# Kernel optimization log

Measured on AMD Instinct MI355X. Metric: run time of the kernel, lower is better.

## Reference

```python
import jax, jax.numpy as jnp
import numpy as np

B, C, H, T = 20, 395, 10, 8192  # batch, input channels, hidden, seq len
GATE_IN = 2 * C + H             # = 800, matches Linear(800, 10)
INIT_IN = 87                    # initilaizer = Linear(87, hidden)


def _uni(k, shape, fan_in):
    s = 1.0 / np.sqrt(fan_in)
    return jax.random.uniform(k, shape, jnp.float32, -s, s)


def setup_inputs() -> dict:
    key = jax.random.key(0)
    ks = jax.random.split(key, 12)
    x = jax.random.normal(ks[0], (B, C, T), jnp.float32)
    y = jax.random.normal(ks[1], (B, C, T), jnp.float32)
    Wf = _uni(ks[2], (H, GATE_IN), GATE_IN); bf = _uni(ks[3], (H,), GATE_IN)
    Wi = _uni(ks[4], (H, GATE_IN), GATE_IN); bi = _uni(ks[5], (H,), GATE_IN)
    Wu = _uni(ks[6], (H, GATE_IN), GATE_IN); bu = _uni(ks[7], (H,), GATE_IN)
    Wo = _uni(ks[8], (H, GATE_IN), GATE_IN); bo = _uni(ks[9], (H,), GATE_IN)
    W_init = _uni(ks[10], (H, INIT_IN), INIT_IN); b_init = _uni(ks[11], (H,), INIT_IN)
    return dict(x=x, y=y, Wf=Wf, bf=bf, Wi=Wi, bi=bi, Wu=Wu, bu=bu,
                Wo=Wo, bo=bo, W_init=W_init, b_init=b_init)


def reference(x, y, Wf, bf, Wi, bi, Wu, bu, Wo, bo, W_init, b_init):
    b_, c_, t_ = x.shape
    h_ = Wf.shape[0]
    # initial states: h0 zeros; c0 = Linear(87->H)(zeros(20,87)) == broadcast bias
    h0 = jnp.zeros((b_, h_), x.dtype)
    c0 = jnp.zeros((b_, INIT_IN), x.dtype) @ W_init.T + b_init  # (B, H)
    # y_prev[t] = y[t-1], zeros at t=0
    y_prev = jnp.concatenate([jnp.zeros((b_, c_, 1), x.dtype), y[..., :-1]], axis=-1)
    # stacked input per step is [x_t, h, y_prev]; split weights accordingly
    W = jnp.stack([Wf, Wi, Wu, Wo])           # (4, H, 2C+H)
    bvec = jnp.stack([bf, bi, bu, bo])        # (4, H)
    Wx, Wh, Wy = W[..., :c_], W[..., c_:c_ + h_], W[..., c_ + h_:]
    # precompute all input-dependent gate pre-activations: (T, B, 4, H)
    pre = (jnp.einsum('bct,ghc->tbgh', x, Wx)
           + jnp.einsum('bct,ghc->tbgh', y_prev, Wy)
           + bvec)

    def step(carry, pre_t):
        h, c = carry
        z = pre_t + jnp.einsum('bh,goh->bgo', h, Wh)  # (B, 4, H)
        f = jax.nn.sigmoid(z[:, 0])
        i = jax.nn.sigmoid(z[:, 1])
        g = jnp.tanh(z[:, 2])
        o = jax.nn.sigmoid(z[:, 3])
        c = c * f + i * g
        h = o * jnp.tanh(c)
        return (h, c), h

    (_, cT), hs = jax.lax.scan(step, (h0, c0), pre)  # hs: (T, B, H)
    out = jnp.moveaxis(hs, 0, -1)  # (B, H, T), matches torch.stack(..., dim=-1)
    return out, cT
```

## Files before the change

kernel.cpp:

```cpp
#include <hip/hip_runtime.h>

#define Bn 20
#define Cn 395
#define Hn 10
#define Tn 8192
#define TP (Tn + 8)
#define GIN 800
#define CP 400
#define NL2E (-1.4426950408889634f)

__global__ __launch_bounds__(256) void pclstm_wt(
    const float* __restrict__ Wf, const float* __restrict__ Wi,
    const float* __restrict__ Wu, const float* __restrict__ Wo,
    float* __restrict__ wt)
{
  int i = blockIdx.x * 256 + threadIdx.x;
  if (i >= CP * 80) return;
  int c = i / 80;
  int q = i - c * 80;
  float v = 0.f;
  if (c < Cn) {
    int qq = (q < 40) ? q : q - 40;
    int h = qq >> 2;
    int g = qq & 3;
    const float* W = (g == 0) ? Wf : (g == 1) ? Wi : (g == 2) ? Wu : Wo;
    float s = (g == 2) ? 2.f * NL2E : NL2E;
    int col = (q < 40) ? c : (Cn + Hn + c);
    v = W[h * GIN + col] * s;
  }
  wt[i] = v;
}

#define SC 80
#define NSTAGE (CP / SC)

__global__ __launch_bounds__(256) void pclstm_pre(
    const float* __restrict__ x, const float* __restrict__ y,
    const float* __restrict__ wt, float* __restrict__ pre)
{
  __shared__ float4 wls[SC * 20];

  const int tid = threadIdx.x;
  const int b = blockIdx.y;
  const int t = blockIdx.x * 256 + tid;

  const float* xb = x + (size_t)b * Cn * Tn + t;
  const float* yb = y + (size_t)b * Cn * Tn + ((t > 0) ? t - 1 : 0);
  const float ym = (t > 0) ? 1.f : 0.f;

  float acc[40];
#pragma unroll
  for (int q = 0; q < 40; ++q) acc[q] = 0.f;

  float xr[8], yr[8];
#pragma unroll
  for (int d = 0; d < 8; ++d) {
    xr[d] = xb[(size_t)d * Tn];
    yr[d] = ym * yb[(size_t)d * Tn];
  }

  const float4* wt4 = reinterpret_cast<const float4*>(wt);

  for (int s = 0; s < NSTAGE; ++s) {
    __syncthreads();
#pragma unroll
    for (int i = 0; i < 7; ++i) {
      int idx = i * 256 + tid;
      if (idx < SC * 20) wls[idx] = wt4[(size_t)s * (SC * 20) + idx];
    }
    __syncthreads();

#pragma unroll 8
    for (int cc = 0; cc < SC; ++cc) {
      const int c = s * SC + cc;
      const int slot = cc & 7;
      float xv = xr[slot];
      float yv = yr[slot];
      int cp = c + 8;
      cp = (cp < Cn) ? cp : (Cn - 1);
      xr[slot] = xb[(size_t)cp * Tn];
      yr[slot] = ym * yb[(size_t)cp * Tn];

      const float4* wr4 = &wls[cc * 20];
#pragma unroll
      for (int k = 0; k < 10; ++k) {
        float4 wx = wr4[k];
        float4 wy = wr4[k + 10];
        acc[4*k+0] = fmaf(xv, wx.x, acc[4*k+0]);
        acc[4*k+1] = fmaf(xv, wx.y, acc[4*k+1]);
        acc[4*k+2] = fmaf(xv, wx.z, acc[4*k+2]);
        acc[4*k+3] = fmaf(xv, wx.w, acc[4*k+3]);
        acc[4*k+0] = fmaf(yv, wy.x, acc[4*k+0]);
        acc[4*k+1] = fmaf(yv, wy.y, acc[4*k+1]);
        acc[4*k+2] = fmaf(yv, wy.z, acc[4*k+2]);
        acc[4*k+3] = fmaf(yv, wy.w, acc[4*k+3]);
      }
    }
  }

  float4* dst = reinterpret_cast<float4*>(pre + ((size_t)b * TP + t) * 40);
#pragma unroll
  for (int k = 0; k < 10; ++k) {
    float4 v4;
    v4.x = acc[4*k+0]; v4.y = acc[4*k+1]; v4.z = acc[4*k+2]; v4.w = acc[4*k+3];
    dst[k] = v4;
  }
}

#define QP(v, ctrl) __int_as_float(__builtin_amdgcn_update_dpp( \
    0, __float_as_int(v), (ctrl), 0xf, 0xf, true))

__global__ __launch_bounds__(64) void pclstm_scan(
    const float* __restrict__ pre,
    const float* __restrict__ Wf, const float* __restrict__ Wi,
    const float* __restrict__ Wu, const float* __restrict__ Wo,
    const float* __restrict__ bfp, const float* __restrict__ bip,
    const float* __restrict__ bup, const float* __restrict__ bop,
    const float* __restrict__ b_init,
    float* __restrict__ out)
{
  const int b = blockIdx.x;
  const int l = threadIdx.x;
  const int lc = (l < 40) ? l : 39;
  const int o = lc >> 2;
  const int g = lc & 3;

  const float* W  = (g == 0) ? Wf : (g == 1) ? Wi : (g == 2) ? Wu : Wo;
  const float* bp = (g == 0) ? bfp : (g == 1) ? bip : (g == 2) ? bup : bop;
  const float sg  = (g == 2) ? 2.f * NL2E : NL2E;
  const float ag  = (g == 2) ? 2.f : 1.f;
  const float bgc = (g == 2) ? -1.f : 0.f;

  float wh[10];
#pragma unroll
  for (int j = 0; j < 10; ++j) wh[j] = W[o * GIN + Cn + j] * sg;
  const float sgb = sg * bp[o];

  const float* preb = pre + (size_t)b * TP * 40 + lc;
  float c = b_init[o];
  float h = 0.f;
  float hb[10];
#pragma unroll
  for (int j = 0; j < 10; ++j) hb[j] = 0.f;

  float pbuf[8];
#pragma unroll
  for (int k = 0; k < 8; ++k) pbuf[k] = preb[(size_t)k * 40];

  const bool sl = (l < 40) && (g == 3);
  float* outb = out + (size_t)b * Hn * Tn;
  float hs[4];

#pragma unroll 8
  for (int t = 0; t < Tn; ++t) {
    float pv = pbuf[t & 7];
    pbuf[t & 7] = preb[(size_t)(t + 8) * 40];

    float pvs = pv + sgb;

    float m1 = wh[2] * hb[2];
    float m2 = wh[4] * hb[4];
    float m3 = wh[6] * hb[6];
    float m4 = wh[8] * hb[8];
    float s0 = fmaf(wh[0], hb[0], pvs);
    float s1 = fmaf(wh[1], hb[1], m1);
    float s2 = fmaf(wh[3], hb[3], m2);
    float s3 = fmaf(wh[5], hb[5], m3);
    float s4 = fmaf(wh[7], hb[7], m4);
    s0 = fmaf(wh[9], hb[9], s0);
    float zs = (s0 + s1) + (s2 + (s3 + s4));

    float e = __builtin_amdgcn_exp2f(zs);
    float r = __builtin_amdgcn_rcpf(1.f + e);
    float gate = fmaf(ag, r, bgc);

    float fv = QP(gate, 0x00);
    float iv = QP(gate, 0x55);
    float uv = QP(gate, 0xAA);
    float ov = QP(gate, 0xFF);

    c = fmaf(c, fv, iv * uv);
    float zc = (2.f * NL2E) * c;
    float e2 = __builtin_amdgcn_exp2f(zc);
    float r2 = __builtin_amdgcn_rcpf(1.f + e2);
    float th = fmaf(2.f, r2, -1.f);
    h = ov * th;

    hs[t & 3] = h;
    if (((t & 3) == 3) && sl) {
      float4 v4; v4.x = hs[0]; v4.y = hs[1]; v4.z = hs[2]; v4.w = hs[3];
      *reinterpret_cast<float4*>(outb + (size_t)o * Tn + t - 3) = v4;
    }

#pragma unroll
    for (int j = 0; j < 10; ++j)
      hb[j] = __int_as_float(__builtin_amdgcn_readlane(__float_as_int(h), 4 * j));
  }
  if ((l < 40) && (g == 0)) out[(size_t)Bn * Hn * Tn + b * Hn + o] = c;
}

extern "C" void kernel_launch(void* const* d_in, const int* in_sizes, int n_in,
                              void* d_out, int out_size, void* d_ws, size_t ws_size,
                              hipStream_t stream) {
  const float* x      = (const float*)d_in[0];
  const float* y      = (const float*)d_in[1];
  const float* Wf     = (const float*)d_in[2];
  const float* bf     = (const float*)d_in[3];
  const float* Wi     = (const float*)d_in[4];
  const float* bi     = (const float*)d_in[5];
  const float* Wu     = (const float*)d_in[6];
  const float* bu     = (const float*)d_in[7];
  const float* Wo     = (const float*)d_in[8];
  const float* bo     = (const float*)d_in[9];
  const float* b_init = (const float*)d_in[11];
  float* out = (float*)d_out;

  float* wt  = (float*)d_ws;
  float* pre = (float*)((char*)d_ws + 131072);

  pclstm_wt<<<(CP * 80 + 255) / 256, 256, 0, stream>>>(Wf, Wi, Wu, Wo, wt);
  dim3 g1(Tn / 256, Bn);
  pclstm_pre<<<g1, 256, 0, stream>>>(x, y, wt, pre);
  pclstm_scan<<<Bn, 64, 0, stream>>>(pre, Wf, Wi, Wu, Wo, bf, bi, bu, bo, b_init, out);
}
```

Before: 1.427 ms.

## Fuse projection and scan into one kernel with flag-based producer/consumer overlap

```diff
diff --git a/kernel.cpp b/kernel.cpp
--- a/kernel.cpp
+++ b/kernel.cpp
@@ -8,13 +8,20 @@
 #define GIN 800
 #define CP 400
 #define NL2E (-1.4426950408889634f)
-
-__global__ __launch_bounds__(256) void pclstm_wt(
+#define KC (2.f * NL2E)
+
+#define SUBT 128
+#define NSUB (Tn / SUBT)
+#define PREBLK (NSUB * Bn)
+#define NFLAGS (Bn * NSUB)
+
+__global__ __launch_bounds__(256) void pclstm_setup(
     const float* __restrict__ Wf, const float* __restrict__ Wi,
     const float* __restrict__ Wu, const float* __restrict__ Wo,
-    float* __restrict__ wt)
+    float* __restrict__ wt, int* __restrict__ flags)
 {
   int i = blockIdx.x * 256 + threadIdx.x;
+  if (i < NFLAGS) flags[i] = 0;
   if (i >= CP * 80) return;
   int c = i / 80;
   int q = i - c * 80;
@@ -31,87 +38,13 @@
   wt[i] = v;
 }
 
-#define SC 80
-#define NSTAGE (CP / SC)
-
-__global__ __launch_bounds__(256) void pclstm_pre(
-    const float* __restrict__ x, const float* __restrict__ y,
-    const float* __restrict__ wt, float* __restrict__ pre)
-{
-  __shared__ float4 wls[SC * 20];
-
-  const int tid = threadIdx.x;
-  const int b = blockIdx.y;
-  const int t = blockIdx.x * 256 + tid;
-
-  const float* xb = x + (size_t)b * Cn * Tn + t;
-  const float* yb = y + (size_t)b * Cn * Tn + ((t > 0) ? t - 1 : 0);
-  const float ym = (t > 0) ? 1.f : 0.f;
-
-  float acc[40];
-#pragma unroll
-  for (int q = 0; q < 40; ++q) acc[q] = 0.f;
-
-  float xr[8], yr[8];
-#pragma unroll
-  for (int d = 0; d < 8; ++d) {
-    xr[d] = xb[(size_t)d * Tn];
-    yr[d] = ym * yb[(size_t)d * Tn];
-  }
-
-  const float4* wt4 = reinterpret_cast<const float4*>(wt);
-
-  for (int s = 0; s < NSTAGE; ++s) {
-    __syncthreads();
-#pragma unroll
-    for (int i = 0; i < 7; ++i) {
-      int idx = i * 256 + tid;
-      if (idx < SC * 20) wls[idx] = wt4[(size_t)s * (SC * 20) + idx];
-    }
-    __syncthreads();
-
-#pragma unroll 8
-    for (int cc = 0; cc < SC; ++cc) {
-      const int c = s * SC + cc;
-      const int slot = cc & 7;
-      float xv = xr[slot];
-      float yv = yr[slot];
-      int cp = c + 8;
-      cp = (cp < Cn) ? cp : (Cn - 1);
-      xr[slot] = xb[(size_t)cp * Tn];
-      yr[slot] = ym * yb[(size_t)cp * Tn];
-
-      const float4* wr4 = &wls[cc * 20];
-#pragma unroll
-      for (int k = 0; k < 10; ++k) {
-        float4 wx = wr4[k];
-        float4 wy = wr4[k + 10];
-        acc[4*k+0] = fmaf(xv, wx.x, acc[4*k+0]);
-        acc[4*k+1] = fmaf(xv, wx.y, acc[4*k+1]);
-        acc[4*k+2] = fmaf(xv, wx.z, acc[4*k+2]);
-        acc[4*k+3] = fmaf(xv, wx.w, acc[4*k+3]);
-        acc[4*k+0] = fmaf(yv, wy.x, acc[4*k+0]);
-        acc[4*k+1] = fmaf(yv, wy.y, acc[4*k+1]);
-        acc[4*k+2] = fmaf(yv, wy.z, acc[4*k+2]);
-        acc[4*k+3] = fmaf(yv, wy.w, acc[4*k+3]);
-      }
-    }
-  }
-
-  float4* dst = reinterpret_cast<float4*>(pre + ((size_t)b * TP + t) * 40);
-#pragma unroll
-  for (int k = 0; k < 10; ++k) {
-    float4 v4;
-    v4.x = acc[4*k+0]; v4.y = acc[4*k+1]; v4.z = acc[4*k+2]; v4.w = acc[4*k+3];
-    dst[k] = v4;
-  }
-}
-
 #define QP(v, ctrl) __int_as_float(__builtin_amdgcn_update_dpp( \
     0, __float_as_int(v), (ctrl), 0xf, 0xf, true))
 
-__global__ __launch_bounds__(64) void pclstm_scan(
-    const float* __restrict__ pre,
+__global__ __launch_bounds__(128) void pclstm_fused(
+    const float* __restrict__ x, const float* __restrict__ y,
+    const float* __restrict__ wt, float* __restrict__ pre,
+    int* __restrict__ flags,
     const float* __restrict__ Wf, const float* __restrict__ Wi,
     const float* __restrict__ Wu, const float* __restrict__ Wo,
     const float* __restrict__ bfp, const float* __restrict__ bip,
@@ -119,84 +52,173 @@
     const float* __restrict__ b_init,
     float* __restrict__ out)
 {
-  const int b = blockIdx.x;
-  const int l = threadIdx.x;
-  const int lc = (l < 40) ? l : 39;
-  const int o = lc >> 2;
-  const int g = lc & 3;
+  __shared__ float4 wls[200 * 20];
+
+  const int bid = blockIdx.x;
+  const int tid = threadIdx.x;
+
+  if (bid >= Bn) {
+    const int i = bid - Bn;
+    const int sub = i / Bn;
+    const int b = i - sub * Bn;
+    const int t = sub * SUBT + tid;
+
+    const float* xb = x + (size_t)b * Cn * Tn + t;
+    const float* yb = y + (size_t)b * Cn * Tn + ((t > 0) ? t - 1 : 0);
+    const float ym = (t > 0) ? 1.f : 0.f;
+
+    float acc[40];
+#pragma unroll
+    for (int q = 0; q < 40; ++q) acc[q] = 0.f;
+
+    float xr[8], yr[8];
+#pragma unroll
+    for (int d = 0; d < 8; ++d) {
+      xr[d] = xb[(size_t)d * Tn];
+      yr[d] = ym * yb[(size_t)d * Tn];
+    }
+
+    const float4* wt4 = reinterpret_cast<const float4*>(wt);
+
+    for (int half = 0; half < 2; ++half) {
+      __syncthreads();
+      for (int j = tid; j < 4000; j += 128)
+        wls[j] = wt4[half * 4000 + j];
+      __syncthreads();
+
+#pragma unroll 8
+      for (int cc = 0; cc < 200; ++cc) {
+        const int c = half * 200 + cc;
+        const int slot = cc & 7;
+        float xv = xr[slot], yv = yr[slot];
+        int cp = c + 8;
+        cp = (cp < Cn) ? cp : (Cn - 1);
+        xr[slot] = xb[(size_t)cp * Tn];
+        yr[slot] = ym * yb[(size_t)cp * Tn];
+
+        const float4* wr4 = &wls[cc * 20];
+#pragma unroll
+        for (int k = 0; k < 10; ++k) {
+          float4 wx = wr4[k];
+          float4 wy = wr4[k + 10];
+          acc[4*k+0] = fmaf(xv, wx.x, acc[4*k+0]);
+          acc[4*k+1] = fmaf(xv, wx.y, acc[4*k+1]);
+          acc[4*k+2] = fmaf(xv, wx.z, acc[4*k+2]);
+          acc[4*k+3] = fmaf(xv, wx.w, acc[4*k+3]);
+          acc[4*k+0] = fmaf(yv, wy.x, acc[4*k+0]);
+          acc[4*k+1] = fmaf(yv, wy.y, acc[4*k+1]);
+          acc[4*k+2] = fmaf(yv, wy.z, acc[4*k+2]);
+          acc[4*k+3] = fmaf(yv, wy.w, acc[4*k+3]);
+        }
+      }
+    }
+
+    float4* dst = reinterpret_cast<float4*>(pre + ((size_t)b * TP + t) * 40);
+#pragma unroll
+    for (int k = 0; k < 10; ++k) {
+      float4 v4;
+      v4.x = acc[4*k+0]; v4.y = acc[4*k+1]; v4.z = acc[4*k+2]; v4.w = acc[4*k+3];
+      dst[k] = v4;
+    }
+
+    __syncthreads();
+    if (tid == 0)
+      __hip_atomic_store(&flags[b * NSUB + sub], 1,
+                         __ATOMIC_RELEASE, __HIP_MEMORY_SCOPE_AGENT);
+    return;
+  }
+
+  if (tid >= 40) return;
+  const int b = bid;
+  const int l = tid;
+  const int o = l >> 2;
+  const int g = l & 3;
 
   const float* W  = (g == 0) ? Wf : (g == 1) ? Wi : (g == 2) ? Wu : Wo;
   const float* bp = (g == 0) ? bfp : (g == 1) ? bip : (g == 2) ? bup : bop;
   const float sg  = (g == 2) ? 2.f * NL2E : NL2E;
-  const float ag  = (g == 2) ? 2.f : 1.f;
-  const float bgc = (g == 2) ? -1.f : 0.f;
+  const float ag  = (g == 2) ? 2.f * KC : 1.f;
+  const float bgc = (g == 2) ? -KC : 0.f;
 
   float wh[10];
 #pragma unroll
   for (int j = 0; j < 10; ++j) wh[j] = W[o * GIN + Cn + j] * sg;
   const float sgb = sg * bp[o];
 
-  const float* preb = pre + (size_t)b * TP * 40 + lc;
-  float c = b_init[o];
+  int* fb = flags + b * NSUB;
+  const float* preb = pre + (size_t)b * TP * 40 + l;
+  float cs = KC * b_init[o];
   float h = 0.f;
   float hb[10];
 #pragma unroll
   for (int j = 0; j < 10; ++j) hb[j] = 0.f;
 
+  while (__hip_atomic_load(&fb[0], __ATOMIC_ACQUIRE, __HIP_MEMORY_SCOPE_AGENT) == 0)
+    __builtin_amdgcn_s_sleep(2);
+
   float pbuf[8];
 #pragma unroll
   for (int k = 0; k < 8; ++k) pbuf[k] = preb[(size_t)k * 40];
 
-  const bool sl = (l < 40) && (g == 3);
+  const bool sl = (g == 3);
   float* outb = out + (size_t)b * Hn * Tn;
-  float hs[4];
-
+  float hs[8];
+
+  for (int ts = 0; ts < NSUB; ++ts) {
+    if (ts + 1 < NSUB) {
+      while (__hip_atomic_load(&fb[ts + 1], __ATOMIC_ACQUIRE,
+                               __HIP_MEMORY_SCOPE_AGENT) == 0)
+        __builtin_amdgcn_s_sleep(2);
+    }
 #pragma unroll 8
-  for (int t = 0; t < Tn; ++t) {
-    float pv = pbuf[t & 7];
-    pbuf[t & 7] = preb[(size_t)(t + 8) * 40];
-
-    float pvs = pv + sgb;
-
-    float m1 = wh[2] * hb[2];
-    float m2 = wh[4] * hb[4];
-    float m3 = wh[6] * hb[6];
-    float m4 = wh[8] * hb[8];
-    float s0 = fmaf(wh[0], hb[0], pvs);
-    float s1 = fmaf(wh[1], hb[1], m1);
-    float s2 = fmaf(wh[3], hb[3], m2);
-    float s3 = fmaf(wh[5], hb[5], m3);
-    float s4 = fmaf(wh[7], hb[7], m4);
-    s0 = fmaf(wh[9], hb[9], s0);
-    float zs = (s0 + s1) + (s2 + (s3 + s4));
-
-    float e = __builtin_amdgcn_exp2f(zs);
-    float r = __builtin_amdgcn_rcpf(1.f + e);
-    float gate = fmaf(ag, r, bgc);
-
-    float fv = QP(gate, 0x00);
-    float iv = QP(gate, 0x55);
-    float uv = QP(gate, 0xAA);
-    float ov = QP(gate, 0xFF);
-
-    c = fmaf(c, fv, iv * uv);
-    float zc = (2.f * NL2E) * c;
-    float e2 = __builtin_amdgcn_exp2f(zc);
-    float r2 = __builtin_amdgcn_rcpf(1.f + e2);
-    float th = fmaf(2.f, r2, -1.f);
-    h = ov * th;
-
-    hs[t & 3] = h;
-    if (((t & 3) == 3) && sl) {
-      float4 v4; v4.x = hs[0]; v4.y = hs[1]; v4.z = hs[2]; v4.w = hs[3];
-      *reinterpret_cast<float4*>(outb + (size_t)o * Tn + t - 3) = v4;
-    }
-
-#pragma unroll
-    for (int j = 0; j < 10; ++j)
-      hb[j] = __int_as_float(__builtin_amdgcn_readlane(__float_as_int(h), 4 * j));
+    for (int tt = 0; tt < SUBT; ++tt) {
+      const int t = (ts << 7) + tt;
+      float pv = pbuf[tt & 7] + sgb;
+      pbuf[tt & 7] = preb[(size_t)(t + 8) * 40];
+
+      float m1 = wh[2] * hb[2];
+      float m2 = wh[4] * hb[4];
+      float m3 = wh[6] * hb[6];
+      float m4 = wh[8] * hb[8];
+      float s0 = fmaf(wh[0], hb[0], pv);
+      float s1 = fmaf(wh[1], hb[1], m1);
+      float s2 = fmaf(wh[3], hb[3], m2);
+      float s3 = fmaf(wh[5], hb[5], m3);
+      float s4 = fmaf(wh[7], hb[7], m4);
+      s0 = fmaf(wh[9], hb[9], s0);
+      float zs = (s0 + s1) + (s2 + (s3 + s4));
+
+      float e = __builtin_amdgcn_exp2f(zs);
+      float r = __builtin_amdgcn_rcpf(1.f + e);
+      float gate = fmaf(ag, r, bgc);
+
+      float fv = QP(gate, 0x00);
+      float iv = QP(gate, 0x55);
+      float uv = QP(gate, 0xAA);
+      float ov = QP(gate, 0xFF);
+
+      float ov2 = ov + ov;
+      float ovn = -ov;
+      cs = fmaf(cs, fv, iv * uv);
+      float e2 = __builtin_amdgcn_exp2f(cs);
+      float r2 = __builtin_amdgcn_rcpf(1.f + e2);
+      h = fmaf(ov2, r2, ovn);
+
+      hs[tt & 7] = h;
+      if (((tt & 7) == 7) && sl) {
+        float4 v4; v4.x = hs[0]; v4.y = hs[1]; v4.z = hs[2]; v4.w = hs[3];
+        float4 w4; w4.x = hs[4]; w4.y = hs[5]; w4.z = hs[6]; w4.w = hs[7];
+        float* p = outb + (size_t)o * Tn + t - 7;
+        *reinterpret_cast<float4*>(p) = v4;
+        *reinterpret_cast<float4*>(p + 4) = w4;
+      }
+
+#pragma unroll
+      for (int j = 0; j < 10; ++j)
+        hb[j] = __int_as_float(__builtin_amdgcn_readlane(__float_as_int(h), 4 * j));
+    }
   }
-  if ((l < 40) && (g == 0)) out[(size_t)Bn * Hn * Tn + b * Hn + o] = c;
+  if (g == 0) out[(size_t)Bn * Hn * Tn + b * Hn + o] = cs * (1.f / KC);
 }
 
 extern "C" void kernel_launch(void* const* d_in, const int* in_sizes, int n_in,
@@ -215,11 +237,12 @@
   const float* b_init = (const float*)d_in[11];
   float* out = (float*)d_out;
 
-  float* wt  = (float*)d_ws;
-  float* pre = (float*)((char*)d_ws + 131072);
-
-  pclstm_wt<<<(CP * 80 + 255) / 256, 256, 0, stream>>>(Wf, Wi, Wu, Wo, wt);
-  dim3 g1(Tn / 256, Bn);
-  pclstm_pre<<<g1, 256, 0, stream>>>(x, y, wt, pre);
-  pclstm_scan<<<Bn, 64, 0, stream>>>(pre, Wf, Wi, Wu, Wo, bf, bi, bu, bo, b_init, out);
+  const size_t PRE_B = (size_t)Bn * TP * 40 * 4;
+  float* wt    = (float*)d_ws;
+  float* pre   = (float*)((char*)d_ws + 131072);
+  int*   flags = (int*)((char*)d_ws + 131072 + PRE_B);
+
+  pclstm_setup<<<(CP * 80 + 255) / 256, 256, 0, stream>>>(Wf, Wi, Wu, Wo, wt, flags);
+  pclstm_fused<<<Bn + PREBLK, 128, 0, stream>>>(
+      x, y, wt, pre, flags, Wf, Wi, Wu, Wo, bf, bi, bu, bo, b_init, out);
 }
```

Measured after the change: 1.572 ms. 1.1x slower.
